# Kernel tuning notes

Hardware: AMD Instinct MI355X
Metric: run time of the kernel (lower is better)

Reference implementation:

```python
import jax, jax.numpy as jnp
import numpy as np

B = 32
H = 56
WD = 56
C = 192
NH = 6
WS = 7   # window size
SS = 3   # shift size
HID = 4 * C
N = WS * WS
NW = (H // WS) * (WD // WS)


def _rel_pos_index():
    coords = np.stack(np.meshgrid(np.arange(WS), np.arange(WS), indexing='ij'))  # [2,ws,ws]
    cf = coords.reshape(2, -1)
    rel = cf[:, :, None] - cf[:, None, :]          # [2,N,N]
    rel = rel.transpose(1, 2, 0)
    rel[..., 0] += WS - 1
    rel[..., 1] += WS - 1
    rel[..., 0] *= 2 * WS - 1
    return rel.sum(-1)                              # [N,N] int


def _attn_mask():
    img = np.zeros((H, WD))
    sl = (slice(0, -WS), slice(-WS, -SS), slice(-SS, None))
    cnt = 0
    for hs in sl:
        for ws in sl:
            img[hs, ws] = cnt
            cnt += 1
    mw = img.reshape(H // WS, WS, WD // WS, WS).transpose(0, 2, 1, 3).reshape(-1, N)  # [nW,N]
    d = mw[:, None, :] - mw[:, :, None]
    return np.where(d != 0, -100.0, 0.0).astype(np.float32)  # [nW,N,N]


_RPI = jnp.asarray(_rel_pos_index())
_MASK = jnp.asarray(_attn_mask())


def setup_inputs() -> dict:
    key = jax.random.key(0)
    ks = jax.random.split(key, 8)
    s = 0.02
    return {
        'x': jax.random.normal(ks[0], (B, H * WD, C), jnp.float32),
        'norm1_g': jnp.ones((C,), jnp.float32),
        'norm1_b': jnp.zeros((C,), jnp.float32),
        'qkv_w': jax.random.normal(ks[1], (C, 3 * C), jnp.float32) * s,
        'qkv_b': jnp.zeros((3 * C,), jnp.float32),
        'rel_bias': jax.random.normal(ks[2], ((2 * WS - 1) ** 2, NH), jnp.float32) * s,
        'proj_w': jax.random.normal(ks[3], (C, C), jnp.float32) * s,
        'proj_b': jnp.zeros((C,), jnp.float32),
        'norm2_g': jnp.ones((C,), jnp.float32),
        'norm2_b': jnp.zeros((C,), jnp.float32),
        'fc1_w': jax.random.normal(ks[4], (C, HID), jnp.float32) * s,
        'fc1_b': jnp.zeros((HID,), jnp.float32),
        'fc2_w': jax.random.normal(ks[5], (HID, C), jnp.float32) * s,
        'fc2_b': jnp.zeros((C,), jnp.float32),
    }


def _ln(x, g, b, eps=1e-5):
    m = jnp.mean(x, axis=-1, keepdims=True)
    v = jnp.mean(jnp.square(x - m), axis=-1, keepdims=True)
    return (x - m) / jnp.sqrt(v + eps) * g + b


def reference(x, norm1_g, norm1_b, qkv_w, qkv_b, rel_bias, proj_w, proj_b,
              norm2_g, norm2_b, fc1_w, fc1_b, fc2_w, fc2_b):
    hd = C // NH
    shortcut = x
    xn = _ln(x, norm1_g, norm1_b).reshape(B, H, WD, C)
    xs = jnp.roll(xn, (-SS, -SS), axis=(1, 2))                     # cyclic shift
    # window partition -> [B*nW, N, C]
    xw = xs.reshape(B, H // WS, WS, WD // WS, WS, C)
    xw = xw.transpose(0, 1, 3, 2, 4, 5).reshape(-1, N, C)
    # windowed attention
    qkv = (xw @ qkv_w + qkv_b).reshape(-1, N, 3, NH, hd).transpose(2, 0, 3, 1, 4)
    q, k, v = qkv[0], qkv[1], qkv[2]                               # [B*nW, NH, N, hd]
    attn = jnp.einsum('whnd,whmd->whnm', q * (hd ** -0.5), k)      # [B*nW, NH, N, N]
    bias = rel_bias[_RPI.reshape(-1)].reshape(N, N, NH).transpose(2, 0, 1)
    attn = attn + bias[None]
    attn = attn.reshape(B, NW, NH, N, N) + _MASK[None, :, None]
    attn = jax.nn.softmax(attn.reshape(-1, NH, N, N), axis=-1)
    out = jnp.einsum('whnm,whmd->whnd', attn, v)
    out = out.transpose(0, 2, 1, 3).reshape(-1, N, C)
    out = out @ proj_w + proj_b
    # window reverse + un-shift
    out = out.reshape(B, H // WS, WD // WS, WS, WS, C)
    out = out.transpose(0, 1, 3, 2, 4, 5).reshape(B, H, WD, C)
    out = jnp.roll(out, (SS, SS), axis=(1, 2)).reshape(B, H * WD, C)
    x = shortcut + out
    # MLP (exact GELU, matching torch nn.GELU default)
    xm = _ln(x, norm2_g, norm2_b)
    h = jax.nn.gelu(xm @ fc1_w + fc1_b, approximate=False)
    return x + (h @ fc2_w + fc2_b)
```

## Files before the change

kernel.cpp:

```cpp
#include <hip/hip_runtime.h>
#include <math.h>


constexpr long T = 100352;

typedef __attribute__((ext_vector_type(8))) short short8;
typedef __attribute__((ext_vector_type(4))) float f32x4;

__device__ __forceinline__ short bf16(float f) {
    union { float f; unsigned u; } v; v.f = f;
    return (short)((v.u + 0x7fff + ((v.u >> 16) & 1)) >> 16);
}

template<int K, int N>
__global__ __launch_bounds__(256)
void pack_k(const float* __restrict__ W, short* __restrict__ P)
{
    const int idx = blockIdx.x * 256 + threadIdx.x;
    const int k = idx / N, n = idx - k * N;
    constexpr int Kst = K / 32;
    const int flat = (((n >> 4) * Kst + (k >> 5)) * 64 +
                      (((k >> 3) & 3) << 4) + (n & 15)) * 8 + (k & 7);
    P[flat] = bf16(W[idx]);
}

__global__ __launch_bounds__(256)
void pack_fc2_k(const float* __restrict__ W, short* __restrict__ P)
{
    const int idx = blockIdx.x * 256 + threadIdx.x;
    const int k = idx / 192, n = idx - k * 192;
    const int t = k >> 6, ks = (k >> 5) & 1, nt = n >> 4;
    const int flat = ((((t * 12 + nt) << 1) + ks) * 64 +
                      (((k >> 3) & 3) << 4) + (n & 15)) * 8 + (k & 7);
    P[flat] = bf16(W[idx]);
}

__global__ __launch_bounds__(256)
void pack_proj_k(const float* __restrict__ W, short* __restrict__ P)
{
    const int idx = blockIdx.x * 256 + threadIdx.x;
    const int k = idx / 192, n = idx - k * 192;
    const int ks = k >> 5, nt = n >> 4;
    const int flat = (((ks * 12 + nt) * 64) +
                      (((k >> 3) & 3) << 4) + (n & 15)) * 8 + (k & 7);
    P[flat] = bf16(W[idx]);
}

__global__ __launch_bounds__(256)
void biasprep_k(const float* __restrict__ relb, float* __restrict__ bm)
{
    const int idx = blockIdx.x * 256 + threadIdx.x;
    if (idx >= 6 * 4 * 2401) return;
    const int e = idx % 2401, rest = idx / 2401;
    const int tw = rest & 1, th = (rest >> 1) & 1, head = rest >> 2;
    const int i = e / 49, j = e - i * 49;
    const int yi = i / 7, xi = i - yi * 7, yj = j / 7, xj = j - yj * 7;
    const float v = relb[((yi - yj + 6) * 13 + (xi - xj + 6)) * 6 + head];
    const int hi = th ? 49 + yi : yi, hj = th ? 49 + yj : yj;
    const int wa = tw ? 49 + xi : xi, wb = tw ? 49 + xj : xj;
    const int Li = (hi < 49 ? 0 : (hi < 53 ? 1 : 2)) * 3 + (wa < 49 ? 0 : (wa < 53 ? 1 : 2));
    const int Lj = (hj < 49 ? 0 : (hj < 53 ? 1 : 2)) * 3 + (wb < 49 ? 0 : (wb < 53 ? 1 : 2));
    bm[idx] = (Li != Lj) ? v - 100.0f : v;
}

__global__ __launch_bounds__(256)
void lnstats_k(const float* __restrict__ x, float* __restrict__ mean,
               float* __restrict__ rstd)
{
    const int wave = threadIdx.x >> 6;
    const int lane = threadIdx.x & 63;
    const long tok = (long)blockIdx.x * 4 + wave;
    const float* p = x + tok * 192;
    const float a = p[lane], b = p[lane + 64], c = p[lane + 128];
    float s = a + b + c;
    float q = a * a + b * b + c * c;
    #pragma unroll
    for (int off = 32; off > 0; off >>= 1) {
        s += __shfl_xor(s, off);
        q += __shfl_xor(q, off);
    }
    if (lane == 0) {
        const float m = s * (1.0f / 192.0f);
        const float v = q * (1.0f / 192.0f) - m * m;
        mean[tok] = m;
        rstd[tok] = 1.0f / sqrtf(v + 1e-5f);
    }
}

__global__ __launch_bounds__(256)
void winattn_k(const float* __restrict__ x, const float* __restrict__ n1g,
               const float* __restrict__ n1b, const short* __restrict__ qkvP,
               const float* __restrict__ qkv_b, const float* __restrict__ bm,
               const float* __restrict__ mean, const float* __restrict__ rstd,
               float* __restrict__ outp)
{
    __shared__ __align__(16) short Kf[6][2048];
    __shared__ __align__(16) short Vf[6][2048];
    __shared__ __align__(16) short Pf[4][1024];
    const int bw  = blockIdx.x;
    const int tid = threadIdx.x;
    const int b = bw >> 6, wi = bw & 63, wh = wi >> 3, ww = wi & 7;
    const int wave = tid >> 6, lane = tid & 63;
    const int col = lane & 15, rbase = (lane >> 4) << 2;
    const float scale = 0.17677669529663687f;

    const int am = lane & 15;
    const int arow = (wave << 4) + am;
    const int kof = (lane >> 4) << 3;
    short8 afr[6];
    long tokA = 0; float mA = 0.f, rsA = 1.f;
    const bool avalid = arow < 49;
    if (avalid) {
        const int yi = arow / 7, xi = arow - yi * 7;
        int h = wh * 7 + yi + 3; if (h >= 56) h -= 56;
        int w = ww * 7 + xi + 3; if (w >= 56) w -= 56;
        tokA = (long)b * 3136 + h * 56 + w;
        mA = mean[tokA]; rsA = rstd[tokA];
    }
    #pragma unroll
    for (int ks = 0; ks < 6; ++ks) {
        short8 a = {};
        if (avalid) {
            const int k0 = (ks << 5) + kof;
            const float4 v0 = *(const float4*)(x + tokA * 192 + k0);
            const float4 v1 = *(const float4*)(x + tokA * 192 + k0 + 4);
            const float4 g0 = *(const float4*)(n1g + k0);
            const float4 g1 = *(const float4*)(n1g + k0 + 4);
            const float4 e0 = *(const float4*)(n1b + k0);
            const float4 e1 = *(const float4*)(n1b + k0 + 4);
            a[0] = bf16((v0.x - mA) * rsA * g0.x + e0.x);
            a[1] = bf16((v0.y - mA) * rsA * g0.y + e0.y);
            a[2] = bf16((v0.z - mA) * rsA * g0.z + e0.z);
            a[3] = bf16((v0.w - mA) * rsA * g0.w + e0.w);
            a[4] = bf16((v1.x - mA) * rsA * g1.x + e1.x);
            a[5] = bf16((v1.y - mA) * rsA * g1.y + e1.y);
            a[6] = bf16((v1.z - mA) * rsA * g1.z + e1.z);
            a[7] = bf16((v1.w - mA) * rsA * g1.w + e1.w);
        }
        afr[ks] = a;
    }

    short8 qfrag[6];
    #pragma unroll
    for (int nt = 0; nt < 12; ++nt) {
        f32x4 acc = {};
        #pragma unroll
        for (int ks = 0; ks < 6; ++ks) {
            const short8 bfr = *(const short8*)(qkvP + ((nt * 6 + ks) * 64 + lane) * 8);
            acc = __builtin_amdgcn_mfma_f32_16x16x32_bf16(afr[ks], bfr, acc, 0, 0, 0);
        }
        const int hh = nt >> 1, d = ((nt & 1) << 4) + col;
        const float bias = qkv_b[hh * 32 + d];
        #pragma unroll
        for (int r = 0; r < 4; ++r) {
            const int m = rbase + r;
            Pf[wave][((m + (((d >> 3) & 3) << 4)) << 3) + (d & 7)] =
                bf16((acc[r] + bias) * scale);
        }
        if (nt & 1) qfrag[hh] = *(const short8*)&Pf[wave][lane << 3];
    }
    #pragma unroll
    for (int nt = 0; nt < 12; ++nt) {
        f32x4 acc = {};
        #pragma unroll
        for (int ks = 0; ks < 6; ++ks) {
            const short8 bfr = *(const short8*)(qkvP + (((nt + 12) * 6 + ks) * 64 + lane) * 8);
            acc = __builtin_amdgcn_mfma_f32_16x16x32_bf16(afr[ks], bfr, acc, 0, 0, 0);
        }
        const int hh = nt >> 1, d = ((nt & 1) << 4) + col;
        const float bias = qkv_b[192 + hh * 32 + d];
        #pragma unroll
        for (int r = 0; r < 4; ++r) {
            const int m = rbase + r;
            Kf[hh][(((wave << 6) + m + (((d >> 3) & 3) << 4)) << 3) + (d & 7)] =
                bf16(acc[r] + bias);
        }
    }
    #pragma unroll
    for (int nt = 0; nt < 12; ++nt) {
        f32x4 acc = {};
        #pragma unroll
        for (int ks = 0; ks < 6; ++ks) {
            const short8 bfr = *(const short8*)(qkvP + (((nt + 24) * 6 + ks) * 64 + lane) * 8);
            acc = __builtin_amdgcn_mfma_f32_16x16x32_bf16(afr[ks], bfr, acc, 0, 0, 0);
        }
        const int hh = nt >> 1, dt = nt & 1, d = (dt << 4) + col;
        const float bias = qkv_b[384 + hh * 32 + d];
        #pragma unroll
        for (int r = 0; r < 4; ++r) {
            const int m = rbase + r;
            const int flat = ((((dt << 1) + (wave >> 1)) << 6) + col +
                              ((((wave << 1) + (m >> 3)) & 3) << 4)) * 8 + (m & 7);
            Vf[hh][flat] = bf16(acc[r] + bias);
        }
    }
    __syncthreads();

    long tok_r[4]; bool iv[4]; int i49[4];
    #pragma unroll
    for (int r = 0; r < 4; ++r) {
        const int i = (wave << 4) + rbase + r;
        iv[r] = i < 49;
        i49[r] = iv[r] ? i * 49 : 0;
        if (iv[r]) {
            const int yi = i / 7, xi = i - yi * 7;
            int h = wh * 7 + yi + 3; if (h >= 56) h -= 56;
            int w = ww * 7 + xi + 3; if (w >= 56) w -= 56;
            tok_r[r] = (long)b * 3136 + h * 56 + w;
        } else tok_r[r] = 0;
    }

    for (int h = 0; h < 6; ++h) {
        const float* bmp = bm + (((h << 1) + (wh == 7)) * 2 + (ww == 7)) * 2401;
        f32x4 sa[4];
        #pragma unroll
        for (int jt = 0; jt < 4; ++jt) {
            f32x4 z = {};
            const short8 kfr = *(const short8*)&Kf[h][((jt << 6) + lane) << 3];
            sa[jt] = __builtin_amdgcn_mfma_f32_16x16x32_bf16(qfrag[h], kfr, z, 0, 0, 0);
        }
        float p[4][4];
        #pragma unroll
        for (int jt = 0; jt < 4; ++jt) {
            const int j = (jt << 4) + col;
            #pragma unroll
            for (int r = 0; r < 4; ++r)
                p[jt][r] = (j < 49) ? sa[jt][r] + bmp[i49[r] + j] : -1e30f;
        }
        #pragma unroll
        for (int r = 0; r < 4; ++r) {
            float mx = fmaxf(fmaxf(p[0][r], p[1][r]), fmaxf(p[2][r], p[3][r]));
            mx = fmaxf(mx, __shfl_xor(mx, 1));
            mx = fmaxf(mx, __shfl_xor(mx, 2));
            mx = fmaxf(mx, __shfl_xor(mx, 4));
            mx = fmaxf(mx, __shfl_xor(mx, 8));
            float sum = 0.f;
            #pragma unroll
            for (int jt = 0; jt < 4; ++jt) {
                const float e = (((jt << 4) + col) < 49) ? __expf(p[jt][r] - mx) : 0.f;
                p[jt][r] = e; sum += e;
            }
            sum += __shfl_xor(sum, 1);
            sum += __shfl_xor(sum, 2);
            sum += __shfl_xor(sum, 4);
            sum += __shfl_xor(sum, 8);
            const float inv = 1.0f / sum;
            #pragma unroll
            for (int jt = 0; jt < 4; ++jt) p[jt][r] *= inv;
        }
        #pragma unroll
        for (int jt = 0; jt < 4; ++jt) {
            #pragma unroll
            for (int r = 0; r < 4; ++r) {
                const int m = rbase + r;
                const int flat = (((jt >> 1) << 6) + m +
                                  ((((jt & 1) << 1) + (col >> 3)) << 4)) * 8 + (col & 7);
                Pf[wave][flat] = bf16(p[jt][r]);
            }
        }
        const short8 p0 = *(const short8*)&Pf[wave][lane << 3];
        const short8 p1 = *(const short8*)&Pf[wave][(64 + lane) << 3];
        f32x4 oa[2] = {};
        #pragma unroll
        for (int dt = 0; dt < 2; ++dt) {
            const short8 v0 = *(const short8*)&Vf[h][(((dt << 1) << 6) + lane) << 3];
            const short8 v1 = *(const short8*)&Vf[h][((((dt << 1) + 1) << 6) + lane) << 3];
            oa[dt] = __builtin_amdgcn_mfma_f32_16x16x32_bf16(p0, v0, oa[dt], 0, 0, 0);
            oa[dt] = __builtin_amdgcn_mfma_f32_16x16x32_bf16(p1, v1, oa[dt], 0, 0, 0);
        }
        #pragma unroll
        for (int dt = 0; dt < 2; ++dt)
            #pragma unroll
            for (int r = 0; r < 4; ++r)
                if (iv[r])
                    outp[tok_r[r] * 192 + h * 32 + (dt << 4) + col] = oa[dt][r];
    }
}

__global__ __launch_bounds__(256, 2)
void projmlp_k(const float* attnb, const short* __restrict__ projP,
               const float* __restrict__ pb, const float* __restrict__ x,
               const float* __restrict__ n2g, const float* __restrict__ n2b,
               const short* __restrict__ fc1P, const float* __restrict__ b1,
               const short* __restrict__ fc2P, const float* __restrict__ b2,
               float* outp)
{
    __shared__ __align__(16) short S1[12288];
    __shared__ __align__(16) short S2[12288];
    __shared__ __align__(16) short Xf[12288];
    __shared__ __align__(16) short Hs[4096];
    const int tid = threadIdx.x;
    const int wave = tid >> 6, lane = tid & 63;
    const int col = lane & 15, rbase = (lane >> 4) << 2;
    const int kof = (lane >> 4) << 3;
    const long m0 = (long)blockIdx.x * 64;

    const long arow = m0 + (wave << 4) + col;
    const float* ap = attnb + arow * 192;
    short8 afr[6];
    #pragma unroll
    for (int ks = 0; ks < 6; ++ks) {
        const int k0 = (ks << 5) + kof;
        const float4 v0 = *(const float4*)(ap + k0);
        const float4 v1 = *(const float4*)(ap + k0 + 4);
        short8 a;
        a[0] = bf16(v0.x); a[1] = bf16(v0.y); a[2] = bf16(v0.z); a[3] = bf16(v0.w);
        a[4] = bf16(v1.x); a[5] = bf16(v1.y); a[6] = bf16(v1.z); a[7] = bf16(v1.w);
        afr[ks] = a;
    }
    f32x4 x1a[12] = {};
    #pragma unroll
    for (int ks = 0; ks < 6; ++ks) {
        #pragma unroll
        for (int nt = 0; nt < 12; ++nt) {
            const short8 bfr = *(const short8*)(projP + ks * 6144 + (nt << 9) + (lane << 3));
            x1a[nt] = __builtin_amdgcn_mfma_f32_16x16x32_bf16(afr[ks], bfr, x1a[nt], 0, 0, 0);
        }
    }
    const long orow = m0 + (wave << 4) + rbase;
    #pragma unroll
    for (int nt = 0; nt < 12; ++nt) {
        const int n = (nt << 4) + col;
        const float bias = pb[n];
        #pragma unroll
        for (int r = 0; r < 4; ++r)
            x1a[nt][r] += bias + x[(orow + r) * 192 + n];
    }
    float s0 = 0.f, s1_ = 0.f, s2_ = 0.f, s3 = 0.f;
    float q0 = 0.f, q1 = 0.f, q2 = 0.f, q3 = 0.f;
    #pragma unroll
    for (int nt = 0; nt < 12; ++nt) {
        s0 += x1a[nt][0]; q0 += x1a[nt][0] * x1a[nt][0];
        s1_ += x1a[nt][1]; q1 += x1a[nt][1] * x1a[nt][1];
        s2_ += x1a[nt][2]; q2 += x1a[nt][2] * x1a[nt][2];
        s3 += x1a[nt][3]; q3 += x1a[nt][3] * x1a[nt][3];
    }
    #pragma unroll
    for (int off = 8; off > 0; off >>= 1) {
        s0 += __shfl_xor(s0, off); q0 += __shfl_xor(q0, off);
        s1_ += __shfl_xor(s1_, off); q1 += __shfl_xor(q1, off);
        s2_ += __shfl_xor(s2_, off); q2 += __shfl_xor(q2, off);
        s3 += __shfl_xor(s3, off); q3 += __shfl_xor(q3, off);
    }
    float mr[4], rr[4];
    mr[0] = s0 * (1.0f / 192.0f); rr[0] = rsqrtf(q0 * (1.0f / 192.0f) - mr[0] * mr[0] + 1e-5f);
    mr[1] = s1_ * (1.0f / 192.0f); rr[1] = rsqrtf(q1 * (1.0f / 192.0f) - mr[1] * mr[1] + 1e-5f);
    mr[2] = s2_ * (1.0f / 192.0f); rr[2] = rsqrtf(q2 * (1.0f / 192.0f) - mr[2] * mr[2] + 1e-5f);
    mr[3] = s3 * (1.0f / 192.0f); rr[3] = rsqrtf(q3 * (1.0f / 192.0f) - mr[3] * mr[3] + 1e-5f);
    short* Xw = Xf + wave * 3072;
    #pragma unroll
    for (int nt = 0; nt < 12; ++nt) {
        const int k = (nt << 4) + col;
        const float g = n2g[k], bb = n2b[k];
        #pragma unroll
        for (int r = 0; r < 4; ++r) {
            const int row16 = rbase + r;
            const int flat = (((k >> 5) << 6) + (((k >> 3) & 3) << 4) + row16) * 8 + (k & 7);
            Xw[flat] = bf16((x1a[nt][r] - mr[r]) * rr[r] * g + bb);
        }
    }

    const short8* f1p = (const short8*)fc1P;
    const short8* f2p = (const short8*)fc2P;
    short8 R1[6], R2[6];
    #pragma unroll
    for (int i = 0; i < 6; ++i) {
        R1[i] = f1p[tid + (i << 8)];
        R2[i] = f2p[tid + (i << 8)];
    }
    short* Hw = Hs + wave * 1024;
    f32x4 accO[12] = {};
    for (int t = 0; t < 12; ++t) {
        __syncthreads();
        #pragma unroll
        for (int i = 0; i < 6; ++i) {
            ((short8*)S1)[tid + (i << 8)] = R1[i];
            ((short8*)S2)[tid + (i << 8)] = R2[i];
        }
        __syncthreads();
        if (t < 11) {
            const short8* n1p = f1p + (t + 1) * 1536;
            const short8* n2p = f2p + (t + 1) * 1536;
            #pragma unroll
            for (int i = 0; i < 6; ++i) {
                R1[i] = n1p[tid + (i << 8)];
                R2[i] = n2p[tid + (i << 8)];
            }
        }
        f32x4 accH[4] = {};
        #pragma unroll
        for (int ks = 0; ks < 6; ++ks) {
            const short8 a = *(const short8*)(Xw + (((ks << 6) + lane) << 3));
            #pragma unroll
            for (int nt = 0; nt < 4; ++nt) {
                const short8 bfr = *(const short8*)&S1[((nt * 6 + ks) << 9) + (lane << 3)];
                accH[nt] = __builtin_amdgcn_mfma_f32_16x16x32_bf16(a, bfr, accH[nt], 0, 0, 0);
            }
        }
        #pragma unroll
        for (int nt = 0; nt < 4; ++nt) {
            const int kh = (nt << 4) + col;
            const float bias = b1[(t << 6) + kh];
            #pragma unroll
            for (int r = 0; r < 4; ++r) {
                const int m = rbase + r;
                float val = accH[nt][r] + bias;
                val = 0.5f * val * (1.0f + erff(val * 0.7071067811865476f));
                const int flat = (((kh >> 5) << 6) + (((kh >> 3) & 3) << 4) + m) * 8 + (kh & 7);
                Hw[flat] = bf16(val);
            }
        }
        #pragma unroll
        for (int ks = 0; ks < 2; ++ks) {
            const short8 a = *(const short8*)(Hw + (((ks << 6) + lane) << 3));
            #pragma unroll
            for (int nt = 0; nt < 12; ++nt) {
                const short8 bfr = *(const short8*)&S2[(((nt << 1) + ks) << 9) + (lane << 3)];
                accO[nt] = __builtin_amdgcn_mfma_f32_16x16x32_bf16(a, bfr, accO[nt], 0, 0, 0);
            }
        }
    }

    #pragma unroll
    for (int nt = 0; nt < 12; ++nt) {
        const int n = (nt << 4) + col;
        const float bias = b2[n];
        #pragma unroll
        for (int r = 0; r < 4; ++r)
            outp[(orow + r) * 192 + n] = accO[nt][r] + bias + x1a[nt][r];
    }
}

extern "C" void kernel_launch(void* const* d_in, const int* in_sizes, int n_in,
                              void* d_out, int out_size, void* d_ws, size_t ws_size,
                              hipStream_t stream)
{
    const float* x      = (const float*)d_in[0];
    const float* n1g    = (const float*)d_in[1];
    const float* n1b    = (const float*)d_in[2];
    const float* qkv_w  = (const float*)d_in[3];
    const float* qkv_b  = (const float*)d_in[4];
    const float* relb   = (const float*)d_in[5];
    const float* proj_w = (const float*)d_in[6];
    const float* proj_b = (const float*)d_in[7];
    const float* n2g    = (const float*)d_in[8];
    const float* n2b    = (const float*)d_in[9];
    const float* fc1_w  = (const float*)d_in[10];
    const float* fc1_b  = (const float*)d_in[11];
    const float* fc2_w  = (const float*)d_in[12];
    const float* fc2_b  = (const float*)d_in[13];
    float* out = (float*)d_out;
    char*  ws  = (char*)d_ws;

    float* mb    = (float*)(ws);
    float* rb    = (float*)(ws +   401408L);
    short* qkvP  = (short*)(ws +   802816L);
    short* projP = (short*)(ws +  1024000L);
    short* fc1P  = (short*)(ws +  1097728L);
    short* fc2P  = (short*)(ws +  1392640L);
    float* bmT   = (float*)(ws +  1687552L);

    pack_k<192, 576><<<432, 256, 0, stream>>>(qkv_w, qkvP);
    pack_proj_k<<<144, 256, 0, stream>>>(proj_w, projP);
    pack_k<192, 768><<<576, 256, 0, stream>>>(fc1_w, fc1P);
    pack_fc2_k<<<576, 256, 0, stream>>>(fc2_w, fc2P);
    biasprep_k<<<226, 256, 0, stream>>>(relb, bmT);

    lnstats_k<<<T / 4, 256, 0, stream>>>(x, mb, rb);
    winattn_k<<<2048, 256, 0, stream>>>(x, n1g, n1b, qkvP, qkv_b,
                                        bmT, mb, rb, out);
    projmlp_k<<<T / 64, 256, 0, stream>>>(out, projP, proj_b, x, n2g, n2b,
                                          fc1P, fc1_b, fc2P, fc2_b, out);
}
```

Baseline: 539.3 us.

## Compute K/V per head into double-buffered LDS to cut shared memory and raise occupancy

Instead of computing K and V for all six heads up front into 48KB of LDS, the window attention kernel now computes each head's K and V projection inside the head loop, storing them in a two-slot buffer. This cuts LDS use from about 56KB to 24KB and sets launch bounds to request four blocks per CU. One barrier per head replaces the single barrier, and K/V projection now interleaves with softmax work. It adds per-head synchronization and may raise register pressure under the tighter launch bound.

```diff
diff --git a/kernel.cpp b/kernel.cpp
--- a/kernel.cpp
+++ b/kernel.cpp
@@ -87,15 +87,15 @@
     }
 }
 
-__global__ __launch_bounds__(256)
+__global__ __launch_bounds__(256, 4)
 void winattn_k(const float* __restrict__ x, const float* __restrict__ n1g,
                const float* __restrict__ n1b, const short* __restrict__ qkvP,
                const float* __restrict__ qkv_b, const float* __restrict__ bm,
                const float* __restrict__ mean, const float* __restrict__ rstd,
                float* __restrict__ outp)
 {
-    __shared__ __align__(16) short Kf[6][2048];
-    __shared__ __align__(16) short Vf[6][2048];
+    __shared__ __align__(16) short Kb[2][2048];
+    __shared__ __align__(16) short Vb[2][2048];
     __shared__ __align__(16) short Pf[4][1024];
     const int bw  = blockIdx.x;
     const int tid = threadIdx.x;
@@ -159,42 +159,6 @@
         }
         if (nt & 1) qfrag[hh] = *(const short8*)&Pf[wave][lane << 3];
     }
-    #pragma unroll
-    for (int nt = 0; nt < 12; ++nt) {
-        f32x4 acc = {};
-        #pragma unroll
-        for (int ks = 0; ks < 6; ++ks) {
-            const short8 bfr = *(const short8*)(qkvP + (((nt + 12) * 6 + ks) * 64 + lane) * 8);
-            acc = __builtin_amdgcn_mfma_f32_16x16x32_bf16(afr[ks], bfr, acc, 0, 0, 0);
-        }
-        const int hh = nt >> 1, d = ((nt & 1) << 4) + col;
-        const float bias = qkv_b[192 + hh * 32 + d];
-        #pragma unroll
-        for (int r = 0; r < 4; ++r) {
-            const int m = rbase + r;
-            Kf[hh][(((wave << 6) + m + (((d >> 3) & 3) << 4)) << 3) + (d & 7)] =
-                bf16(acc[r] + bias);
-        }
-    }
-    #pragma unroll
-    for (int nt = 0; nt < 12; ++nt) {
-        f32x4 acc = {};
-        #pragma unroll
-        for (int ks = 0; ks < 6; ++ks) {
-            const short8 bfr = *(const short8*)(qkvP + (((nt + 24) * 6 + ks) * 64 + lane) * 8);
-            acc = __builtin_amdgcn_mfma_f32_16x16x32_bf16(afr[ks], bfr, acc, 0, 0, 0);
-        }
-        const int hh = nt >> 1, dt = nt & 1, d = (dt << 4) + col;
-        const float bias = qkv_b[384 + hh * 32 + d];
-        #pragma unroll
-        for (int r = 0; r < 4; ++r) {
-            const int m = rbase + r;
-            const int flat = ((((dt << 1) + (wave >> 1)) << 6) + col +
-                              ((((wave << 1) + (m >> 3)) & 3) << 4)) * 8 + (m & 7);
-            Vf[hh][flat] = bf16(acc[r] + bias);
-        }
-    }
-    __syncthreads();
 
     long tok_r[4]; bool iv[4]; int i49[4];
     #pragma unroll
@@ -211,12 +175,48 @@
     }
 
     for (int h = 0; h < 6; ++h) {
+        const int bs = h & 1;
+        #pragma unroll
+        for (int half = 0; half < 2; ++half) {
+            const int d = (half << 4) + col;
+            f32x4 acck = {};
+            #pragma unroll
+            for (int ks = 0; ks < 6; ++ks) {
+                const short8 bfr = *(const short8*)(qkvP +
+                    (((12 + 2 * h + half) * 6 + ks) * 64 + lane) * 8);
+                acck = __builtin_amdgcn_mfma_f32_16x16x32_bf16(afr[ks], bfr, acck, 0, 0, 0);
+            }
+            const float biask = qkv_b[192 + h * 32 + d];
+            #pragma unroll
+            for (int r = 0; r < 4; ++r) {
+                const int m = rbase + r;
+                Kb[bs][(((wave << 6) + m + (((d >> 3) & 3) << 4)) << 3) + (d & 7)] =
+                    bf16(acck[r] + biask);
+            }
+            f32x4 accv = {};
+            #pragma unroll
+            for (int ks = 0; ks < 6; ++ks) {
+                const short8 bfr = *(const short8*)(qkvP +
+                    (((24 + 2 * h + half) * 6 + ks) * 64 + lane) * 8);
+                accv = __builtin_amdgcn_mfma_f32_16x16x32_bf16(afr[ks], bfr, accv, 0, 0, 0);
+            }
+            const float biasv = qkv_b[384 + h * 32 + d];
+            #pragma unroll
+            for (int r = 0; r < 4; ++r) {
+                const int m = rbase + r;
+                const int flat = ((((half << 1) + (wave >> 1)) << 6) + col +
+                                  ((((wave << 1) + (m >> 3)) & 3) << 4)) * 8 + (m & 7);
+                Vb[bs][flat] = bf16(accv[r] + biasv);
+            }
+        }
+        __syncthreads();
+
         const float* bmp = bm + (((h << 1) + (wh == 7)) * 2 + (ww == 7)) * 2401;
         f32x4 sa[4];
         #pragma unroll
         for (int jt = 0; jt < 4; ++jt) {
             f32x4 z = {};
-            const short8 kfr = *(const short8*)&Kf[h][((jt << 6) + lane) << 3];
+            const short8 kfr = *(const short8*)&Kb[bs][((jt << 6) + lane) << 3];
             sa[jt] = __builtin_amdgcn_mfma_f32_16x16x32_bf16(qfrag[h], kfr, z, 0, 0, 0);
         }
         float p[4][4];
@@ -263,8 +263,8 @@
         f32x4 oa[2] = {};
         #pragma unroll
         for (int dt = 0; dt < 2; ++dt) {
-            const short8 v0 = *(const short8*)&Vf[h][(((dt << 1) << 6) + lane) << 3];
-            const short8 v1 = *(const short8*)&Vf[h][((((dt << 1) + 1) << 6) + lane) << 3];
+            const short8 v0 = *(const short8*)&Vb[bs][(((dt << 1) << 6) + lane) << 3];
+            const short8 v1 = *(const short8*)&Vb[bs][((((dt << 1) + 1) << 6) + lane) << 3];
             oa[dt] = __builtin_amdgcn_mfma_f32_16x16x32_bf16(p0, v0, oa[dt], 0, 0, 0);
             oa[dt] = __builtin_amdgcn_mfma_f32_16x16x32_bf16(p1, v1, oa[dt], 0, 0, 0);
         }
```

Result: slower. 567.2 us (+5.2%).
